# Kernel optimization log

Measured on AMD Instinct MI355X. Metric: run time of the kernel, lower is better.

Reference implementation:

```python
import jax, jax.numpy as jnp
import numpy as np

N = 1024
E = 16384
F_IN = 128
H = 64
ALPHA = 0.7


def _gcn(x, src, dst, W, b):
    # PyG GCNConv: add self-loops, symmetric deg^{-1/2} normalization, aggregate at dst.
    loop = jnp.arange(N)
    s = jnp.concatenate([src, loop])
    d = jnp.concatenate([dst, loop])
    deg = jax.ops.segment_sum(jnp.ones_like(s, jnp.float32), d, num_segments=N)
    dinv = jnp.where(deg > 0, jax.lax.rsqrt(deg), 0.0)
    norm = dinv[s] * dinv[d]  # [E+N]
    h = x @ W  # [N,H]
    out = jax.ops.segment_sum(norm[:, None] * h[s], d, num_segments=N)
    return out + b


def _gat(x, src, dst, ew, W, a_src, a_dst, w_edge, a_edge, b):
    # PyG GATConv (heads=1) with scalar edge_attr via lin_edge(edge_dim=1).
    h = x @ W  # [N,H]
    al_s = h @ a_src  # [N]
    al_d = h @ a_dst  # [N]
    loop = jnp.arange(N)
    s = jnp.concatenate([src, loop])
    d = jnp.concatenate([dst, loop])
    ew_l = jnp.concatenate([ew, jnp.full((N,), jnp.mean(ew))])  # fill_value='mean' for self-loops
    c = jnp.dot(w_edge, a_edge)  # scalar: (lin_edge(ew) * att_edge).sum() = ew * c
    e = jax.nn.leaky_relu(al_s[s] + al_d[d] + ew_l * c, 0.2)  # [E+N]
    # segment softmax over destination nodes (every node has a self-loop -> no empty segments)
    emax = jax.ops.segment_max(e, d, num_segments=N)
    ex = jnp.exp(e - emax[d])
    denom = jax.ops.segment_sum(ex, d, num_segments=N)
    alpha = ex / denom[d]
    out = jax.ops.segment_sum(alpha[:, None] * h[s], d, num_segments=N)
    return out + b


def setup_inputs() -> dict:
    key = jax.random.key(0)
    ks = jax.random.split(key, 24)
    g = lambda k, shape, fan: jax.random.normal(k, shape, jnp.float32) / np.sqrt(fan)
    inp = {
        "x": jax.random.normal(ks[0], (N, F_IN), jnp.float32),
        "edge_index_above": jax.random.randint(ks[1], (2, E), 0, N),
        "edge_index_distance": jax.random.randint(ks[2], (2, E), 0, N),
        "edge_weights_distance": jax.random.uniform(ks[3], (E,), jnp.float32),
        # GCNConv1 / GATConv1 (in 128 -> 64)
        "W_gcn1": g(ks[4], (F_IN, H), F_IN), "b_gcn1": jnp.zeros((H,), jnp.float32),
        "W_gat1": g(ks[5], (F_IN, H), F_IN), "att_src1": g(ks[6], (H,), H),
        "att_dst1": g(ks[7], (H,), H), "w_edge1": g(ks[8], (H,), 1),
        "att_edge1": g(ks[9], (H,), H), "b_gat1": jnp.zeros((H,), jnp.float32),
        # GCNConv2 / GATConv2 (64 -> 64)
        "W_gcn2": g(ks[10], (H, H), H), "b_gcn2": jnp.zeros((H,), jnp.float32),
        "W_gat2": g(ks[11], (H, H), H), "att_src2": g(ks[12], (H,), H),
        "att_dst2": g(ks[13], (H,), H), "w_edge2": g(ks[14], (H,), 1),
        "att_edge2": g(ks[15], (H,), H), "b_gat2": jnp.zeros((H,), jnp.float32),
        # GCNConv3 (64 -> 64)
        "W_gcn3": g(ks[16], (H, H), H), "b_gcn3": jnp.zeros((H,), jnp.float32),
        # predictor MLP: Linear(128,64) -> ReLU -> Linear(64,1) -> Sigmoid
        "Wp1": g(ks[17], (2 * H, H), 2 * H), "bp1": jnp.zeros((H,), jnp.float32),
        "Wp2": g(ks[18], (H, 1), H), "bp2": jnp.zeros((1,), jnp.float32),
    }
    return inp


def reference(x, edge_index_above, edge_index_distance, edge_weights_distance,
              W_gcn1, b_gcn1, W_gat1, att_src1, att_dst1, w_edge1, att_edge1, b_gat1,
              W_gcn2, b_gcn2, W_gat2, att_src2, att_dst2, w_edge2, att_edge2, b_gat2,
              W_gcn3, b_gcn3, Wp1, bp1, Wp2, bp2):
    sa, da = edge_index_above[0], edge_index_above[1]
    sd, dd = edge_index_distance[0], edge_index_distance[1]
    ew = edge_weights_distance

    xa1 = jax.nn.relu(_gcn(x, sa, da, W_gcn1, b_gcn1))
    xd1 = jax.nn.relu(_gat(x, sd, dd, ew, W_gat1, att_src1, att_dst1, w_edge1, att_edge1, b_gat1))
    xa2 = jax.nn.relu(_gcn(xa1, sa, da, W_gcn2, b_gcn2))
    xd2 = jax.nn.relu(_gat(xd1, sd, dd, ew, W_gat2, att_src2, att_dst2, w_edge2, att_edge2, b_gat2))
    xc = ALPHA * xa2 + (1.0 - ALPHA) * xd2
    h = jax.nn.relu(_gcn(xc, sa, da, W_gcn3, b_gcn3))  # [N,H]

    # All-pairs predictor, fused: concat([h_i, h_j]) @ Wp1 = h_i @ Wp1[:H] + h_j @ Wp1[H:]
    h1 = h @ Wp1[:H]  # [N,H] contribution of start node
    h2 = h @ Wp1[H:]  # [N,H] contribution of end node
    pre = jax.nn.relu(h1[:, None, :] + h2[None, :, :] + bp1)  # [N,N,H]
    logits = jnp.einsum('ijh,h->ij', pre, Wp2[:, 0]) + bp2[0]  # [N,N]
    return jax.nn.sigmoid(logits).reshape(-1)  # [N*N], row-major = cartesian_prod order
```

## Files before the change

### kernel.cpp

```cpp
#include <hip/hip_runtime.h>

constexpr int NV  = 1024;
constexpr int EV  = 16384;
constexpr int FIN = 128;
constexpr int HD  = 64;
constexpr int CAP = 64;

__device__ __forceinline__ float relu_(float v){ return fmaxf(v, 0.f); }

struct KArgs {
    const float* x;
    const int *sa, *da, *sd, *dd;
    const float* ew;
    const float *Wg1, *bg1;
    const float *Wt1, *as1, *ad1, *we1, *ae1, *bt1;
    const float *Wg2, *bg2;
    const float *Wt2, *as2, *ad2, *we2, *ae2, *bt2;
    const float *Wg3, *bg3;
    const float *Wp1, *bp1, *Wp2, *bp2;
    int *cnt_a, *cnt_d;
    float* scal;
    float *al_s1, *al_d1, *al_s2, *al_d2;
    int *ell_a, *ell_d;
    float* ellw_d;
    float *hg1, *hga1, *hg2, *hga2, *hg3, *h1, *h2;
    float* out;
};

__device__ __forceinline__ float gcn_row(const KArgs& A, const float* __restrict__ h,
                                         const float* __restrict__ bias, int d, int k)
{
    int deg = min(A.cnt_a[d], CAP);
    float dv  = rsqrtf((float)deg + 1.f);
    float acc = dv * h[d*HD + k];
    const int* row = A.ell_a + d*CAP;
    int p = 0;
    float a0=0.f, a1=0.f, a2=0.f, a3=0.f;
    for (; p + 4 <= deg; p += 4) {
        int s0=row[p], s1=row[p+1], s2=row[p+2], s3=row[p+3];
        a0 = fmaf(rsqrtf((float)A.cnt_a[s0]+1.f), h[s0*HD + k], a0);
        a1 = fmaf(rsqrtf((float)A.cnt_a[s1]+1.f), h[s1*HD + k], a1);
        a2 = fmaf(rsqrtf((float)A.cnt_a[s2]+1.f), h[s2*HD + k], a2);
        a3 = fmaf(rsqrtf((float)A.cnt_a[s3]+1.f), h[s3*HD + k], a3);
    }
    for (; p < deg; ++p) {
        int s = row[p];
        a0 = fmaf(rsqrtf((float)A.cnt_a[s]+1.f), h[s*HD + k], a0);
    }
    acc += (a0+a1) + (a2+a3);
    return relu_(fmaf(dv, acc, bias[k]));
}

__device__ __forceinline__ float gat_row(const KArgs& A, const float* __restrict__ h,
                                         const float* __restrict__ bias,
                                         float c, float ewm, int d, int k)
{
    int deg = min(A.cnt_d[d], CAP);
    float aD = A.al_d1[0];
    (void)aD;
    return 0.f;
}

template<bool L2>
__device__ __forceinline__ float gat_row_t(const KArgs& A, const float* __restrict__ h,
                                           const float* __restrict__ bias,
                                           const float* __restrict__ al_s,
                                           const float* __restrict__ al_d,
                                           float c, float ewm, int d, int k)
{
    int deg = min(A.cnt_d[d], CAP);
    float aD = al_d[d];
    float es = al_s[d] + aD + ewm*c;
    es = expf((es > 0.f) ? es : 0.2f*es);
    float num = es * h[d*HD + k];
    float den = es;
    const int*   row  = A.ell_d  + d*CAP;
    const float* wrow = A.ellw_d + d*CAP;
    int p = 0;
    for (; p + 2 <= deg; p += 2) {
        int s0 = row[p], s1 = row[p+1];
        float e0 = al_s[s0] + aD + wrow[p]*c;
        float e1 = al_s[s1] + aD + wrow[p+1]*c;
        float x0 = expf((e0 > 0.f) ? e0 : 0.2f*e0);
        float x1 = expf((e1 > 0.f) ? e1 : 0.2f*e1);
        den += x0 + x1;
        num = fmaf(x0, h[s0*HD + k], num);
        num = fmaf(x1, h[s1*HD + k], num);
    }
    for (; p < deg; ++p) {
        int s = row[p];
        float e = al_s[s] + aD + wrow[p]*c;
        float ex = expf((e > 0.f) ? e : 0.2f*e);
        den += ex;
        num = fmaf(ex, h[s*HD + k], num);
    }
    return relu_(num/den + bias[k]);
}

__device__ __forceinline__ float mm_row_lds(const float4* __restrict__ rowF4,
                                            const float* __restrict__ Wf, int j)
{
    float acc = 0.f;
    #pragma unroll
    for (int k4 = 0; k4 < 16; k4++) {
        float4 r = rowF4[k4];
        acc = fmaf(r.x, Wf[(4*k4+0)*64 + j], acc);
        acc = fmaf(r.y, Wf[(4*k4+1)*64 + j], acc);
        acc = fmaf(r.z, Wf[(4*k4+2)*64 + j], acc);
        acc = fmaf(r.w, Wf[(4*k4+3)*64 + j], acc);
    }
    return acc;
}

__global__ __launch_bounds__(256) void k1(KArgs A)
{
    __shared__ __align__(16) float4 Ws[FIN*16];
    const int b = blockIdx.x, tid = threadIdx.x;
    if (b < 512) {
        bool gcn = (b < 256);
        const float4* Wsrc = (const float4*)(gcn ? A.Wg1 : A.Wt1);
        for (int r = tid; r < FIN*16; r += 256) Ws[r] = Wsrc[r];
        __syncthreads();
        int t = (gcn ? b : b-256)*256 + tid, i = t >> 6, j = t & 63;
        const float4* xr = (const float4*)(A.x + i*FIN);
        const float*  Wf = (const float*)Ws;
        float acc = 0.f;
        #pragma unroll
        for (int k4 = 0; k4 < FIN/4; k4++) {
            float4 xv = xr[k4];
            acc = fmaf(xv.x, Wf[(4*k4+0)*64 + j], acc);
            acc = fmaf(xv.y, Wf[(4*k4+1)*64 + j], acc);
            acc = fmaf(xv.z, Wf[(4*k4+2)*64 + j], acc);
            acc = fmaf(xv.w, Wf[(4*k4+3)*64 + j], acc);
        }
        if (gcn) {
            A.hg1[t] = acc;
        } else {
            A.hga1[t] = acc;
            float ps = acc * A.as1[j];
            float pd = acc * A.ad1[j];
            for (int off = 32; off; off >>= 1) {
                ps += __shfl_down(ps, off, 64);
                pd += __shfl_down(pd, off, 64);
            }
            if (j == 0) { A.al_s1[i] = ps; A.al_d1[i] = pd; }
        }
    } else if (b < 576) {
        int e = (b-512)*256 + tid;
        int dA = A.da[e], dD = A.dd[e];
        int pa = atomicAdd(&A.cnt_a[dA], 1);
        if (pa < CAP) A.ell_a[dA*CAP + pa] = A.sa[e];
        float w = A.ew[e];
        int pd = atomicAdd(&A.cnt_d[dD], 1);
        if (pd < CAP) { A.ell_d[dD*CAP + pd] = A.sd[e]; A.ellw_d[dD*CAP + pd] = w; }
        for (int off = 32; off; off >>= 1) w += __shfl_down(w, off, 64);
        if ((tid & 63) == 0) atomicAdd(&A.scal[3], w);
    } else {
        if (tid < 64) {
            float p1 = A.we1[tid]*A.ae1[tid];
            float p2 = A.we2[tid]*A.ae2[tid];
            for (int off = 32; off; off >>= 1) {
                p1 += __shfl_down(p1, off, 64);
                p2 += __shfl_down(p2, off, 64);
            }
            if (tid == 0) { A.scal[1] = p1; A.scal[2] = p2; }
        }
    }
}

__global__ __launch_bounds__(256) void k2(KArgs A)
{
    __shared__ __align__(16) float4 Ws[HD*16];
    __shared__ float rowb[4*64];
    const int b = blockIdx.x, tid = threadIdx.x;
    const float4* Wsrc = (const float4*)((b < 256) ? A.Wg2 : A.Wt2);
    for (int r = tid; r < HD*16; r += 256) Ws[r] = Wsrc[r];
    __syncthreads();
    int w = tid >> 6, k = tid & 63;
    const float* Wf = (const float*)Ws;
    if (b < 256) {
        int d = b*4 + w;
        rowb[w*64 + k] = gcn_row(A, A.hg1, A.bg1, d, k);
        A.hg2[d*HD + k] = mm_row_lds((const float4*)(rowb + w*64), Wf, k);
    } else {
        int i = (b-256)*4 + w;
        float c = A.scal[1], ewm = A.scal[3] * (1.f/EV);
        rowb[w*64 + k] = gat_row_t<false>(A, A.hga1, A.bt1, A.al_s1, A.al_d1,
                                          c, ewm, i, k);
        float acc = mm_row_lds((const float4*)(rowb + w*64), Wf, k);
        A.hga2[i*HD + k] = acc;
        float ps = acc * A.as2[k];
        float pd = acc * A.ad2[k];
        for (int off = 32; off; off >>= 1) {
            ps += __shfl_down(ps, off, 64);
            pd += __shfl_down(pd, off, 64);
        }
        if (k == 0) { A.al_s2[i] = ps; A.al_d2[i] = pd; }
    }
}

__global__ __launch_bounds__(256) void k3(KArgs A)
{
    __shared__ __align__(16) float4 Ws[HD*16];
    __shared__ float rows[4*64];
    const int b = blockIdx.x, tid = threadIdx.x;
    for (int r = tid; r < HD*16; r += 256) Ws[r] = ((const float4*)A.Wg3)[r];
    int w = tid >> 6, k = tid & 63;
    int node = b*2 + (w >> 1);
    float v;
    if ((w & 1) == 0) {
        v = 0.7f * gcn_row(A, A.hg2, A.bg2, node, k);
    } else {
        float c = A.scal[2], ewm = A.scal[3] * (1.f/EV);
        v = 0.3f * gat_row_t<true>(A, A.hga2, A.bt2, A.al_s2, A.al_d2,
                                   c, ewm, node, k);
    }
    rows[w*64 + k] = v;
    __syncthreads();
    if ((w & 1) == 0) {
        const float* Wf = (const float*)Ws;
        const float4* r0 = (const float4*)(rows + w*64);
        const float4* r1 = (const float4*)(rows + (w+1)*64);
        float acc = 0.f;
        #pragma unroll
        for (int k4 = 0; k4 < 16; k4++) {
            float4 ra = r0[k4], rb = r1[k4];
            acc = fmaf(ra.x+rb.x, Wf[(4*k4+0)*64 + k], acc);
            acc = fmaf(ra.y+rb.y, Wf[(4*k4+1)*64 + k], acc);
            acc = fmaf(ra.z+rb.z, Wf[(4*k4+2)*64 + k], acc);
            acc = fmaf(ra.w+rb.w, Wf[(4*k4+3)*64 + k], acc);
        }
        A.hg3[node*HD + k] = acc;
    }
}

__global__ __launch_bounds__(256) void k4(KArgs A)
{
    __shared__ __align__(16) float4 Wp[FIN*16];
    __shared__ float rowb[4*64];
    const int b = blockIdx.x, tid = threadIdx.x;
    for (int r = tid; r < FIN*16; r += 256) Wp[r] = ((const float4*)A.Wp1)[r];
    __syncthreads();
    int w = tid >> 6, k = tid & 63;
    int d = b*4 + w;
    rowb[w*64 + k] = gcn_row(A, A.hg3, A.bg3, d, k);
    const float*  Wf = (const float*)Wp;
    const float4* rF = (const float4*)(rowb + w*64);
    float a1 = 0.f, a2 = 0.f;
    #pragma unroll
    for (int k4i = 0; k4i < 16; k4i++) {
        float4 r = rF[k4i];
        a1 = fmaf(r.x, Wf[(4*k4i+0)*64 + k], a1);
        a2 = fmaf(r.x, Wf[(64+4*k4i+0)*64 + k], a2);
        a1 = fmaf(r.y, Wf[(4*k4i+1)*64 + k], a1);
        a2 = fmaf(r.y, Wf[(64+4*k4i+1)*64 + k], a2);
        a1 = fmaf(r.z, Wf[(4*k4i+2)*64 + k], a1);
        a2 = fmaf(r.z, Wf[(64+4*k4i+2)*64 + k], a2);
        a1 = fmaf(r.w, Wf[(4*k4i+3)*64 + k], a1);
        a2 = fmaf(r.w, Wf[(64+4*k4i+3)*64 + k], a2);
    }
    A.h1[d*HD + k] = a1 + A.bp1[k];
    A.h2[d*HD + k] = a2;
}

__global__ __launch_bounds__(256) void k5(KArgs A)
{
    __shared__ float4 s1[32*17], s2[32*17], w2s[16];
    const int tid = threadIdx.x;
    int by = blockIdx.x >> 5, bx = blockIdx.x & 31;
    int i0 = by*32, j0 = bx*32;
    for (int r = tid; r < 512; r += 256) {
        int row = r >> 4, c = r & 15;
        s1[row*17 + c] = ((const float4*)A.h1)[(i0+row)*16 + c];
        s2[row*17 + c] = ((const float4*)A.h2)[(j0+row)*16 + c];
    }
    if (tid < 16) w2s[tid] = ((const float4*)A.Wp2)[tid];
    __syncthreads();
    int ty = tid >> 4, tx = tid & 15;
    float a00=0.f, a01=0.f, a10=0.f, a11=0.f;
    #pragma unroll
    for (int k4 = 0; k4 < 16; k4++) {
        float4 va0 = s1[ty*17 + k4],      va1 = s1[(ty+16)*17 + k4];
        float4 vb0 = s2[tx*17 + k4],      vb1 = s2[(tx+16)*17 + k4];
        float4 wv  = w2s[k4];
#define STEP(c) \
        a00 = fmaf(fmaxf(va0.c+vb0.c, 0.f), wv.c, a00); \
        a01 = fmaf(fmaxf(va0.c+vb1.c, 0.f), wv.c, a01); \
        a10 = fmaf(fmaxf(va1.c+vb0.c, 0.f), wv.c, a10); \
        a11 = fmaf(fmaxf(va1.c+vb1.c, 0.f), wv.c, a11);
        STEP(x) STEP(y) STEP(z) STEP(w)
#undef STEP
    }
    float bb = A.bp2[0];
    int i = i0 + ty, jj = j0 + tx;
    A.out[i*NV + jj]            = 1.f/(1.f + expf(-(a00+bb)));
    A.out[i*NV + jj + 16]       = 1.f/(1.f + expf(-(a01+bb)));
    A.out[(i+16)*NV + jj]       = 1.f/(1.f + expf(-(a10+bb)));
    A.out[(i+16)*NV + jj + 16]  = 1.f/(1.f + expf(-(a11+bb)));
}

extern "C" void kernel_launch(void* const* d_in, const int* in_sizes, int n_in,
                              void* d_out, int out_size, void* d_ws, size_t ws_size,
                              hipStream_t stream)
{
    KArgs A;
    A.x   = (const float*)d_in[0];
    const int* ei_a = (const int*)d_in[1];
    const int* ei_d = (const int*)d_in[2];
    A.ew  = (const float*)d_in[3];
    A.Wg1 = (const float*)d_in[4];  A.bg1 = (const float*)d_in[5];
    A.Wt1 = (const float*)d_in[6];  A.as1 = (const float*)d_in[7];
    A.ad1 = (const float*)d_in[8];  A.we1 = (const float*)d_in[9];
    A.ae1 = (const float*)d_in[10]; A.bt1 = (const float*)d_in[11];
    A.Wg2 = (const float*)d_in[12]; A.bg2 = (const float*)d_in[13];
    A.Wt2 = (const float*)d_in[14]; A.as2 = (const float*)d_in[15];
    A.ad2 = (const float*)d_in[16]; A.we2 = (const float*)d_in[17];
    A.ae2 = (const float*)d_in[18]; A.bt2 = (const float*)d_in[19];
    A.Wg3 = (const float*)d_in[20]; A.bg3 = (const float*)d_in[21];
    A.Wp1 = (const float*)d_in[22]; A.bp1 = (const float*)d_in[23];
    A.Wp2 = (const float*)d_in[24]; A.bp2 = (const float*)d_in[25];
    A.sa = ei_a;      A.da = ei_a + EV;
    A.sd = ei_d;      A.dd = ei_d + EV;
    A.out = (float*)d_out;

    float* W = (float*)d_ws;
    A.cnt_a  = (int*)(W + 0);
    A.cnt_d  = (int*)(W + 1024);
    A.scal   = W + 2048;
    A.al_s1  = W + 2064;
    A.al_d1  = W + 3088;
    A.al_s2  = W + 4112;
    A.al_d2  = W + 5136;
    A.ell_a  = (int*)(W + 6160);
    A.ell_d  = (int*)(W + 71696);
    A.ellw_d = W + 137232;
    A.hg1    = W + 202768;
    A.hga1   = W + 268304;
    A.hg2    = W + 333840;
    A.hga2   = W + 399376;
    A.hg3    = W + 464912;
    A.h1     = W + 530448;
    A.h2     = W + 595984;

    hipMemsetAsync(d_ws, 0, 2064*sizeof(float), stream);

    k1<<<577,  256, 0, stream>>>(A);
    k2<<<512,  256, 0, stream>>>(A);
    k3<<<512,  256, 0, stream>>>(A);
    k4<<<256,  256, 0, stream>>>(A);
    k5<<<1024, 256, 0, stream>>>(A);
}
```

Measured before the change: 149.8 us.

## Stage transposed padded weights in LDS and enlarge predictor tile to 64x64

Weights are now staged into shared memory transposed, with a padded row stride, so each output column reads contiguous float4 weight vectors instead of strided scalar LDS loads in k1–k4. The all-pairs predictor kernel grows from 32x32 to 64x64 tiles, with a 4x4 register block per thread, which raises arithmetic reuse per LDS load and cuts the block count from 1024 to 256. The transposed staging uses scattered scalar LDS writes. The larger tile uses more registers and leaves fewer blocks to spread across CUs.

```diff
diff --git a/kernel.cpp b/kernel.cpp
--- a/kernel.cpp
+++ b/kernel.cpp
@@ -27,6 +27,20 @@
     float* out;
 };
 
+template<int K>
+__device__ __forceinline__ void stage_wt(const float* __restrict__ W,
+                                         float* __restrict__ Wst, int tid)
+{
+    for (int idx4 = tid; idx4 < K*16; idx4 += 256) {
+        float4 v = ((const float4*)W)[idx4];
+        int k = idx4 >> 4, j4 = (idx4 & 15) * 4;
+        Wst[(j4+0)*(K+4) + k] = v.x;
+        Wst[(j4+1)*(K+4) + k] = v.y;
+        Wst[(j4+2)*(K+4) + k] = v.z;
+        Wst[(j4+3)*(K+4) + k] = v.w;
+    }
+}
+
 __device__ __forceinline__ float gcn_row(const KArgs& A, const float* __restrict__ h,
                                          const float* __restrict__ bias, int d, int k)
 {
@@ -51,17 +65,6 @@
     return relu_(fmaf(dv, acc, bias[k]));
 }
 
-__device__ __forceinline__ float gat_row(const KArgs& A, const float* __restrict__ h,
-                                         const float* __restrict__ bias,
-                                         float c, float ewm, int d, int k)
-{
-    int deg = min(A.cnt_d[d], CAP);
-    float aD = A.al_d1[0];
-    (void)aD;
-    return 0.f;
-}
-
-template<bool L2>
 __device__ __forceinline__ float gat_row_t(const KArgs& A, const float* __restrict__ h,
                                            const float* __restrict__ bias,
                                            const float* __restrict__ al_s,
@@ -97,42 +100,34 @@
     return relu_(num/den + bias[k]);
 }
 
-__device__ __forceinline__ float mm_row_lds(const float4* __restrict__ rowF4,
-                                            const float* __restrict__ Wf, int j)
-{
+template<int K>
+__device__ __forceinline__ float mm_row_wt(const float4* __restrict__ rowF4,
+                                           const float* __restrict__ Wst, int j)
+{
+    const float4* wj = (const float4*)(Wst + j*(K+4));
     float acc = 0.f;
     #pragma unroll
-    for (int k4 = 0; k4 < 16; k4++) {
+    for (int k4 = 0; k4 < K/4; k4++) {
         float4 r = rowF4[k4];
-        acc = fmaf(r.x, Wf[(4*k4+0)*64 + j], acc);
-        acc = fmaf(r.y, Wf[(4*k4+1)*64 + j], acc);
-        acc = fmaf(r.z, Wf[(4*k4+2)*64 + j], acc);
-        acc = fmaf(r.w, Wf[(4*k4+3)*64 + j], acc);
+        float4 w = wj[k4];
+        acc = fmaf(r.x, w.x, acc);
+        acc = fmaf(r.y, w.y, acc);
+        acc = fmaf(r.z, w.z, acc);
+        acc = fmaf(r.w, w.w, acc);
     }
     return acc;
 }
 
 __global__ __launch_bounds__(256) void k1(KArgs A)
 {
-    __shared__ __align__(16) float4 Ws[FIN*16];
+    __shared__ __align__(16) float Wst[64*(FIN+4)];
     const int b = blockIdx.x, tid = threadIdx.x;
     if (b < 512) {
         bool gcn = (b < 256);
-        const float4* Wsrc = (const float4*)(gcn ? A.Wg1 : A.Wt1);
-        for (int r = tid; r < FIN*16; r += 256) Ws[r] = Wsrc[r];
+        stage_wt<FIN>(gcn ? A.Wg1 : A.Wt1, Wst, tid);
         __syncthreads();
         int t = (gcn ? b : b-256)*256 + tid, i = t >> 6, j = t & 63;
-        const float4* xr = (const float4*)(A.x + i*FIN);
-        const float*  Wf = (const float*)Ws;
-        float acc = 0.f;
-        #pragma unroll
-        for (int k4 = 0; k4 < FIN/4; k4++) {
-            float4 xv = xr[k4];
-            acc = fmaf(xv.x, Wf[(4*k4+0)*64 + j], acc);
-            acc = fmaf(xv.y, Wf[(4*k4+1)*64 + j], acc);
-            acc = fmaf(xv.z, Wf[(4*k4+2)*64 + j], acc);
-            acc = fmaf(xv.w, Wf[(4*k4+3)*64 + j], acc);
-        }
+        float acc = mm_row_wt<FIN>((const float4*)(A.x + i*FIN), Wst, j);
         if (gcn) {
             A.hg1[t] = acc;
         } else {
@@ -170,24 +165,22 @@
 
 __global__ __launch_bounds__(256) void k2(KArgs A)
 {
-    __shared__ __align__(16) float4 Ws[HD*16];
+    __shared__ __align__(16) float Wst[64*(HD+4)];
     __shared__ float rowb[4*64];
     const int b = blockIdx.x, tid = threadIdx.x;
-    const float4* Wsrc = (const float4*)((b < 256) ? A.Wg2 : A.Wt2);
-    for (int r = tid; r < HD*16; r += 256) Ws[r] = Wsrc[r];
+    stage_wt<HD>((b < 256) ? A.Wg2 : A.Wt2, Wst, tid);
     __syncthreads();
     int w = tid >> 6, k = tid & 63;
-    const float* Wf = (const float*)Ws;
     if (b < 256) {
         int d = b*4 + w;
         rowb[w*64 + k] = gcn_row(A, A.hg1, A.bg1, d, k);
-        A.hg2[d*HD + k] = mm_row_lds((const float4*)(rowb + w*64), Wf, k);
+        A.hg2[d*HD + k] = mm_row_wt<HD>((const float4*)(rowb + w*64), Wst, k);
     } else {
         int i = (b-256)*4 + w;
         float c = A.scal[1], ewm = A.scal[3] * (1.f/EV);
-        rowb[w*64 + k] = gat_row_t<false>(A, A.hga1, A.bt1, A.al_s1, A.al_d1,
-                                          c, ewm, i, k);
-        float acc = mm_row_lds((const float4*)(rowb + w*64), Wf, k);
+        rowb[w*64 + k] = gat_row_t(A, A.hga1, A.bt1, A.al_s1, A.al_d1,
+                                   c, ewm, i, k);
+        float acc = mm_row_wt<HD>((const float4*)(rowb + w*64), Wst, k);
         A.hga2[i*HD + k] = acc;
         float ps = acc * A.as2[k];
         float pd = acc * A.ad2[k];
@@ -201,10 +194,10 @@
 
 __global__ __launch_bounds__(256) void k3(KArgs A)
 {
-    __shared__ __align__(16) float4 Ws[HD*16];
+    __shared__ __align__(16) float Wst[64*(HD+4)];
     __shared__ float rows[4*64];
     const int b = blockIdx.x, tid = threadIdx.x;
-    for (int r = tid; r < HD*16; r += 256) Ws[r] = ((const float4*)A.Wg3)[r];
+    stage_wt<HD>(A.Wg3, Wst, tid);
     int w = tid >> 6, k = tid & 63;
     int node = b*2 + (w >> 1);
     float v;
@@ -212,23 +205,23 @@
         v = 0.7f * gcn_row(A, A.hg2, A.bg2, node, k);
     } else {
         float c = A.scal[2], ewm = A.scal[3] * (1.f/EV);
-        v = 0.3f * gat_row_t<true>(A, A.hga2, A.bt2, A.al_s2, A.al_d2,
-                                   c, ewm, node, k);
+        v = 0.3f * gat_row_t(A, A.hga2, A.bt2, A.al_s2, A.al_d2,
+                             c, ewm, node, k);
     }
     rows[w*64 + k] = v;
     __syncthreads();
     if ((w & 1) == 0) {
-        const float* Wf = (const float*)Ws;
         const float4* r0 = (const float4*)(rows + w*64);
         const float4* r1 = (const float4*)(rows + (w+1)*64);
+        const float4* wj = (const float4*)(Wst + k*(HD+4));
         float acc = 0.f;
         #pragma unroll
         for (int k4 = 0; k4 < 16; k4++) {
-            float4 ra = r0[k4], rb = r1[k4];
-            acc = fmaf(ra.x+rb.x, Wf[(4*k4+0)*64 + k], acc);
-            acc = fmaf(ra.y+rb.y, Wf[(4*k4+1)*64 + k], acc);
-            acc = fmaf(ra.z+rb.z, Wf[(4*k4+2)*64 + k], acc);
-            acc = fmaf(ra.w+rb.w, Wf[(4*k4+3)*64 + k], acc);
+            float4 ra = r0[k4], rb = r1[k4], wv = wj[k4];
+            acc = fmaf(ra.x+rb.x, wv.x, acc);
+            acc = fmaf(ra.y+rb.y, wv.y, acc);
+            acc = fmaf(ra.z+rb.z, wv.z, acc);
+            acc = fmaf(ra.w+rb.w, wv.w, acc);
         }
         A.hg3[node*HD + k] = acc;
     }
@@ -236,28 +229,26 @@
 
 __global__ __launch_bounds__(256) void k4(KArgs A)
 {
-    __shared__ __align__(16) float4 Wp[FIN*16];
+    __shared__ __align__(16) float Wst[64*(FIN+4)];
     __shared__ float rowb[4*64];
     const int b = blockIdx.x, tid = threadIdx.x;
-    for (int r = tid; r < FIN*16; r += 256) Wp[r] = ((const float4*)A.Wp1)[r];
+    stage_wt<FIN>(A.Wp1, Wst, tid);
     __syncthreads();
     int w = tid >> 6, k = tid & 63;
     int d = b*4 + w;
     rowb[w*64 + k] = gcn_row(A, A.hg3, A.bg3, d, k);
-    const float*  Wf = (const float*)Wp;
     const float4* rF = (const float4*)(rowb + w*64);
+    const float4* wj = (const float4*)(Wst + k*(FIN+4));
     float a1 = 0.f, a2 = 0.f;
     #pragma unroll
     for (int k4i = 0; k4i < 16; k4i++) {
         float4 r = rF[k4i];
-        a1 = fmaf(r.x, Wf[(4*k4i+0)*64 + k], a1);
-        a2 = fmaf(r.x, Wf[(64+4*k4i+0)*64 + k], a2);
-        a1 = fmaf(r.y, Wf[(4*k4i+1)*64 + k], a1);
-        a2 = fmaf(r.y, Wf[(64+4*k4i+1)*64 + k], a2);
-        a1 = fmaf(r.z, Wf[(4*k4i+2)*64 + k], a1);
-        a2 = fmaf(r.z, Wf[(64+4*k4i+2)*64 + k], a2);
-        a1 = fmaf(r.w, Wf[(4*k4i+3)*64 + k], a1);
-        a2 = fmaf(r.w, Wf[(64+4*k4i+3)*64 + k], a2);
+        float4 w1 = wj[k4i];
+        float4 w2 = wj[16 + k4i];
+        a1 = fmaf(r.x, w1.x, a1);  a2 = fmaf(r.x, w2.x, a2);
+        a1 = fmaf(r.y, w1.y, a1);  a2 = fmaf(r.y, w2.y, a2);
+        a1 = fmaf(r.z, w1.z, a1);  a2 = fmaf(r.z, w2.z, a2);
+        a1 = fmaf(r.w, w1.w, a1);  a2 = fmaf(r.w, w2.w, a2);
     }
     A.h1[d*HD + k] = a1 + A.bp1[k];
     A.h2[d*HD + k] = a2;
@@ -265,11 +256,11 @@
 
 __global__ __launch_bounds__(256) void k5(KArgs A)
 {
-    __shared__ float4 s1[32*17], s2[32*17], w2s[16];
+    __shared__ float4 s1[64*17], s2[64*17], w2s[16];
     const int tid = threadIdx.x;
-    int by = blockIdx.x >> 5, bx = blockIdx.x & 31;
-    int i0 = by*32, j0 = bx*32;
-    for (int r = tid; r < 512; r += 256) {
+    int by = blockIdx.x >> 4, bx = blockIdx.x & 15;
+    int i0 = by*64, j0 = bx*64;
+    for (int r = tid; r < 1024; r += 256) {
         int row = r >> 4, c = r & 15;
         s1[row*17 + c] = ((const float4*)A.h1)[(i0+row)*16 + c];
         s2[row*17 + c] = ((const float4*)A.h2)[(j0+row)*16 + c];
@@ -277,26 +268,35 @@
     if (tid < 16) w2s[tid] = ((const float4*)A.Wp2)[tid];
     __syncthreads();
     int ty = tid >> 4, tx = tid & 15;
-    float a00=0.f, a01=0.f, a10=0.f, a11=0.f;
+    float acc[4][4] = {};
     #pragma unroll
     for (int k4 = 0; k4 < 16; k4++) {
-        float4 va0 = s1[ty*17 + k4],      va1 = s1[(ty+16)*17 + k4];
-        float4 vb0 = s2[tx*17 + k4],      vb1 = s2[(tx+16)*17 + k4];
-        float4 wv  = w2s[k4];
-#define STEP(c) \
-        a00 = fmaf(fmaxf(va0.c+vb0.c, 0.f), wv.c, a00); \
-        a01 = fmaf(fmaxf(va0.c+vb1.c, 0.f), wv.c, a01); \
-        a10 = fmaf(fmaxf(va1.c+vb0.c, 0.f), wv.c, a10); \
-        a11 = fmaf(fmaxf(va1.c+vb1.c, 0.f), wv.c, a11);
-        STEP(x) STEP(y) STEP(z) STEP(w)
-#undef STEP
+        float4 va[4], vb[4], wv = w2s[k4];
+        #pragma unroll
+        for (int u = 0; u < 4; u++) {
+            va[u] = s1[(ty + 16*u)*17 + k4];
+            vb[u] = s2[(tx + 16*u)*17 + k4];
+        }
+        #pragma unroll
+        for (int u = 0; u < 4; u++)
+        #pragma unroll
+        for (int v = 0; v < 4; v++) {
+            acc[u][v] = fmaf(fmaxf(va[u].x + vb[v].x, 0.f), wv.x, acc[u][v]);
+            acc[u][v] = fmaf(fmaxf(va[u].y + vb[v].y, 0.f), wv.y, acc[u][v]);
+            acc[u][v] = fmaf(fmaxf(va[u].z + vb[v].z, 0.f), wv.z, acc[u][v]);
+            acc[u][v] = fmaf(fmaxf(va[u].w + vb[v].w, 0.f), wv.w, acc[u][v]);
+        }
     }
     float bb = A.bp2[0];
-    int i = i0 + ty, jj = j0 + tx;
-    A.out[i*NV + jj]            = 1.f/(1.f + expf(-(a00+bb)));
-    A.out[i*NV + jj + 16]       = 1.f/(1.f + expf(-(a01+bb)));
-    A.out[(i+16)*NV + jj]       = 1.f/(1.f + expf(-(a10+bb)));
-    A.out[(i+16)*NV + jj + 16]  = 1.f/(1.f + expf(-(a11+bb)));
+    #pragma unroll
+    for (int u = 0; u < 4; u++) {
+        int i = i0 + ty + 16*u;
+        #pragma unroll
+        for (int v = 0; v < 4; v++) {
+            int jj = j0 + tx + 16*v;
+            A.out[i*NV + jj] = 1.f/(1.f + expf(-(acc[u][v] + bb)));
+        }
+    }
 }
 
 extern "C" void kernel_launch(void* const* d_in, const int* in_sizes, int n_in,
@@ -344,9 +344,9 @@
 
     hipMemsetAsync(d_ws, 0, 2064*sizeof(float), stream);
 
-    k1<<<577,  256, 0, stream>>>(A);
-    k2<<<512,  256, 0, stream>>>(A);
-    k3<<<512,  256, 0, stream>>>(A);
-    k4<<<256,  256, 0, stream>>>(A);
-    k5<<<1024, 256, 0, stream>>>(A);
-}
+    k1<<<577, 256, 0, stream>>>(A);
+    k2<<<512, 256, 0, stream>>>(A);
+    k3<<<512, 256, 0, stream>>>(A);
+    k4<<<256, 256, 0, stream>>>(A);
+    k5<<<256, 256, 0, stream>>>(A);
+}
```

Measured after the change: 153.7 us. +2.6%, slower.
